# Performance work log

Measured on AMD Instinct MI355X. Metric: run time of the kernel, lower is better.

The kernel has to match this reference:

```python
import jax, jax.numpy as jnp
import numpy as np

# Physical constants and grid (match torch WRF.__init__)
PREF = 100000.0
RD = 287.0
G = 9.81
NX, NY, NZ = 384, 384, 48
DX, DY = 1000.0, 1000.0
DZ = 1.0 / (NZ + 1)

# --- staggered-grid stencil primitives (replace F.conv3d with shifts) ---

def pad_x(X):
    # periodic in x
    return jnp.concatenate([X[:, :, -1:], X, X[:, :, :1]], axis=2)

def pad_y(X):
    # periodic in y
    return jnp.concatenate([X[:, -1:, :], X, X[:, :1, :]], axis=1)

def pad_z(X, top=None, surface=None):
    # Dirichlet in z (defaults to zero boundary planes)
    top = top if top is not None else jnp.zeros_like(X[:1])
    surface = surface if surface is not None else jnp.zeros_like(X[:1])
    return jnp.concatenate([top, X, surface], axis=0)

def bar_x(X):
    return (X[:, :, 1:] + X[:, :, :-1]) * 0.5

def bar_y(X):
    return (X[:, 1:, :] + X[:, :-1, :]) * 0.5

def bar_z(X):
    return (X[1:] + X[:-1]) * 0.5

def delta_x(X):
    return (X[:, :, 1:] - X[:, :, :-1]) / DX

def delta_y(X):
    return (X[:, 1:, :] - X[:, :-1, :]) / DY

def delta_z(X):
    return (X[1:] - X[:-1]) / DZ


def rhs(U, V, W, Theta, Mu, Phi, Phi_t, Phi_s, P_t, P_s):
    u = U / bar_x(pad_x(Mu))                      # (NZ, NY, NX+1)
    v = V / bar_y(pad_y(Mu))                      # (NZ, NY+1, NX)
    w = W / bar_z(Mu)                             # (NZ-1, NY, NX)
    alpha = -delta_z(pad_z(Phi, Phi_t, Phi_s)) / Mu   # (NZ, NY, NX)
    theta = Theta / Mu
    p = PREF * (RD * theta / PREF / alpha) ** 1.4
    omega = -w * G / bar_z(alpha) / bar_z(Mu)     # (NZ-1, NY, NX)
    Omega = omega * bar_z(Mu)

    R_U = (-delta_x(bar_x(pad_x(U)) * bar_x(pad_x(u)))
           - delta_y(bar_x(pad_x(V)) * bar_y(pad_y(u)))
           - delta_z(bar_x(pad_x(pad_z(Omega))) * bar_z(pad_z(u))))
    R_V = (-delta_x(bar_y(pad_y(U)) * bar_x(pad_x(v)))
           - delta_y(bar_y(pad_y(V)) * bar_y(pad_y(v)))
           - delta_z(bar_y(pad_y(pad_z(Omega))) * bar_z(pad_z(v))))
    R_W = (-delta_x(bar_z(U) * bar_x(pad_x(w)))
           - delta_y(bar_z(V) * bar_y(pad_y(w)))
           - delta_z(bar_z(pad_z(Omega)) * bar_z(pad_z(w))))
    R_Theta = (-delta_x(U * bar_x(pad_x(theta)))
               - delta_y(V * bar_y(pad_y(theta)))
               - delta_z(pad_z(Omega) * bar_z(pad_z(theta))))
    R_Phi = (-bar_z(bar_x(u)) * delta_x(bar_x(pad_x(Phi)))
             - bar_z(bar_y(v)) * delta_y(bar_y(pad_y(Phi)))
             - omega * delta_z(bar_z(pad_z(Phi, Phi_t, Phi_s))))
    R_Mu = -delta_x(U) - delta_y(V) - delta_z(pad_z(Omega))

    # pressure-gradient terms
    R_U = R_U + (-bar_x(pad_x(Mu)) * bar_x(pad_x(alpha)) * delta_x(pad_x(p))
                 - delta_z(bar_x(bar_z(pad_x(pad_z(p, P_t, P_s)))))
                   * delta_x(pad_x(bar_z(pad_z(Phi, Phi_t, Phi_s)))))
    R_V = R_V + (-bar_y(pad_y(Mu)) * bar_y(pad_y(alpha)) * delta_y(pad_y(p))
                 - delta_z(bar_y(bar_z(pad_y(pad_z(p, P_t, P_s)))))
                   * delta_y(pad_y(bar_z(pad_z(Phi, Phi_t, Phi_s)))))
    R_W = R_W + G * (delta_z(p) - bar_z(Mu))
    R_Phi = R_Phi + G * w
    return R_U, R_V, R_W, R_Theta, R_Mu, R_Phi


def rk3_step(U, V, W, Theta, Mu, Phi, Phi_t, Phi_s, P_t, P_s, dt):
    Uc, Vc, Wc, Tc, Mc, Pc = U, V, W, Theta, Mu, Phi
    for c in (dt / 3.0, dt / 2.0, dt * 1.0):
        rU, rV, rW, rT, rM, rP = rhs(Uc, Vc, Wc, Tc, Mc, Pc, Phi_t, Phi_s, P_t, P_s)
        Uc = U + c * rU
        Vc = V + c * rV
        Wc = W + c * rW
        Tc = Theta + c * rT
        Mc = Mu + c * rM
        Pc = Phi + c * rP
    return (Uc, Vc, Wc, Tc, Mc, Pc)


def setup_inputs() -> dict:
    key = jax.random.key(0)
    k_th, k_u, k_v, k_w = jax.random.split(key, 4)
    # potential temperature with boundary layers, ~300 K
    theta_full = 300.0 + 0.5 * jax.random.normal(k_th, (NZ + 2, NY, NX), dtype=jnp.float32)
    P_t = jnp.zeros((1, NY, NX), dtype=jnp.float32)
    P_s = jnp.full((1, NY, NX), PREF, dtype=jnp.float32)
    # reproduce __init__ hydrostatic setup
    P = jnp.linspace(DZ, 1.0 - DZ, NZ, dtype=jnp.float32).reshape(NZ, 1, 1) * (P_s - P_t) + P_t
    Alpha = RD / PREF * theta_full[1:-1] * (P / PREF) ** (-1.0 / 1.4)
    Mu = jnp.broadcast_to(P_s - P_t, (NZ, NY, NX)).astype(jnp.float32)
    layer = Mu * Alpha * DZ                                  # (NZ, NY, NX)
    # Phi_full[i] = sum_{j>=i} layer[j], Phi_full[NZ] = 0
    Phi_full = jnp.concatenate(
        [jnp.flip(jnp.cumsum(jnp.flip(layer, 0), axis=0), 0),
         jnp.zeros((1, NY, NX), dtype=jnp.float32)], axis=0)  # (NZ+1, NY, NX)
    Phi_t = Phi_full[:1]
    Phi_s = Phi_full[-1:]
    Phi = Phi_full[1:-1]                                     # (NZ-1, NY, NX)
    Theta = theta_full[1:-1] * Mu
    U = 5e5 * jax.random.normal(k_u, (NZ, NY, NX + 1), dtype=jnp.float32)
    V = 5e5 * jax.random.normal(k_v, (NZ, NY + 1, NX), dtype=jnp.float32)
    W = 1e4 * jax.random.normal(k_w, (NZ - 1, NY, NX), dtype=jnp.float32)
    return {"U": U, "V": V, "W": W, "Theta": Theta, "Mu": Mu, "Phi": Phi,
            "Phi_t": Phi_t, "Phi_s": Phi_s, "P_t": P_t, "P_s": P_s, "dt": 4}


def reference(U, V, W, Theta, Mu, Phi, Phi_t, Phi_s, P_t, P_s, dt):
    return rk3_step(U, V, W, Theta, Mu, Phi, Phi_t, Phi_s, P_t, P_s, dt)
```

## Files before the change

kernel.cpp:

```cpp
#include <hip/hip_runtime.h>

namespace {

constexpr int NX = 384, NY = 384, NZ = 48;
constexpr int NXU = NX + 1;
constexpr int PLN = NX * NY;
constexpr float RDX = 1.0f / 1000.0f;
constexpr float RDY = 1.0f / 1000.0f;
constexpr float RDZ = 49.0f;
constexpr float PREF = 100000.0f, RD = 287.0f, G = 9.81f;
constexpr float K_RP = RD / PREF;

constexpr int SZ_U = NZ * NY * NXU;
constexpr int SZ_V = NZ * (NY + 1) * NX;
constexpr int SZ_W = (NZ - 1) * PLN;
constexpr int SZ_T = NZ * PLN;
constexpr int SZ_M = NZ * PLN;
constexpr int SZ_P = (NZ - 1) * PLN;

constexpr int TX = 32, TY = 8;
constexpr int PW = TX + 3;
constexpr int PH = TY + 3;
constexpr int PSZ = PW * PH;
constexpr int KCH = 12, KSPLIT = 4;

struct Idx { int pix, uo, vo, pxa, pxb, pya, pyb; };

__device__ __forceinline__ float frcp(float x) { return __builtin_amdgcn_rcpf(x); }
__device__ __forceinline__ float pow14(float x) {
    return __builtin_amdgcn_exp2f(1.4f * __builtin_amdgcn_logf(x));
}

__global__ __launch_bounds__(256, 3)
void rhs_tile(
    const float* __restrict__ Us, const float* __restrict__ Vs, const float* __restrict__ Ws,
    const float* __restrict__ Ts, const float* __restrict__ Ms, const float* __restrict__ Ps,
    const float* __restrict__ Phit, const float* __restrict__ Phis,
    const float* __restrict__ Pt,   const float* __restrict__ Psrf,
    const float* __restrict__ U0, const float* __restrict__ V0, const float* __restrict__ W0,
    const float* __restrict__ T0, const float* __restrict__ M0, const float* __restrict__ P0,
    float* __restrict__ Uo, float* __restrict__ Vo, float* __restrict__ Wo,
    float* __restrict__ To, float* __restrict__ Mo, float* __restrict__ Po,
    const int* __restrict__ dtp, float coef)
{
    const int tx = threadIdx.x, ty = threadIdx.y;
    const int tid = ty * TX + tx;
    const int i0 = blockIdx.x * TX;
    const int j0 = blockIdx.y * TY;
    const int k0 = blockIdx.z * KCH;
    const int i = i0 + tx, j = j0 + ty;
    const float c = coef * (float)(*dtp);
    const int ly = ty + 1, lx = tx + 1;

    __shared__ float sPH[3][PSZ], sP[3][PSZ], sOM[3][PSZ];
    __shared__ float sAL[2][PSZ], sMU[2][PSZ], sTH[2][PSZ], sUR[2][PSZ], su_[2][PSZ],
                     sVR[2][PSZ], sv_[2][PSZ], sw_[2][PSZ];

    auto mkidx = [&](int idx, Idx& q) {
        const int r  = idx / PW;
        const int cc = idx - r * PW;
        int gj = j0 - 1 + r;  if (gj < 0) gj += NY; else if (gj >= NY) gj -= NY;
        int gi = i0 - 1 + cc; if (gi < 0) gi += NX; else if (gi >= NX) gi -= NX;
        int gII = i0 - 1 + cc; if (gII < 0) gII += NX + 1; else if (gII > NX) gII -= NX + 1;
        int gJJ = j0 - 1 + r;  if (gJJ < 0) gJJ += NY + 1; else if (gJJ > NY) gJJ -= NY + 1;
        q.pix = gj * NX + gi;
        q.uo  = gj * NXU + gII;
        q.vo  = gJJ * NX + gi;
        const int xa = (gII == 0)  ? NX - 1 : gII - 1;
        const int xb = (gII == NX) ? 0      : gII;
        const int ya = (gJJ == 0)  ? NY - 1 : gJJ - 1;
        const int yb = (gJJ == NY) ? 0      : gJJ;
        q.pxa = gj * NX + xa; q.pxb = gj * NX + xb;
        q.pya = ya * NX + gi; q.pyb = yb * NX + gi;
    };
    const bool has2 = (tid + 256 < PSZ);
    Idx q0, q1;
    mkidx(tid, q0);
    mkidx(has2 ? tid + 256 : tid, q1);

    auto fill1 = [&](int l, const Idx& q, int idx) {
        const int s3 = (l + 3) % 3, s2 = l & 1;
        float phv, pv, al = 0.f, th = 0.f, uv = 0.f, vv = 0.f, wv = 0.f, om = 0.f;
        float Uw = 0.f, Vw = 0.f, muw = 0.f;
        if (l >= 0 && l < NZ) {
            phv = (l >= NZ - 1) ? Phis[q.pix] : Ps[l * PLN + q.pix];
            const float phm = (l == 0) ? Phit[q.pix] : Ps[(l - 1) * PLN + q.pix];
            const float mu  = Ms[l * PLN + q.pix];
            const float rmu = frcp(mu);
            al = -(phv - phm) * RDZ * rmu;
            th = Ts[l * PLN + q.pix] * rmu;
            pv = PREF * pow14(K_RP * th * frcp(al));
            const float Uv = Us[l * NY * NXU + q.uo];
            uv = Uv * frcp(0.5f * (Ms[l * PLN + q.pxa] + Ms[l * PLN + q.pxb]));
            const float Vv = Vs[l * (NY + 1) * NX + q.vo];
            vv = Vv * frcp(0.5f * (Ms[l * PLN + q.pya] + Ms[l * PLN + q.pyb]));
            Uw = Uv; Vw = Vv; muw = mu;
            if (l < NZ - 1) {
                const float mu1 = Ms[(l + 1) * PLN + q.pix];
                const float Wv  = Ws[l * PLN + q.pix];
                const float ph1 = (l + 1 >= NZ - 1) ? Phis[q.pix] : Ps[(l + 1) * PLN + q.pix];
                const float al1 = -(ph1 - phv) * RDZ * frcp(mu1);
                const float mz  = 0.5f * (mu + mu1);
                wv = Wv * frcp(mz);
                om = -Wv * G * frcp(0.5f * (al + al1) * mz);
            }
        } else {
            phv = (l < 0) ? Phit[q.pix] : Phis[q.pix];
            pv  = (l < 0) ? Pt[q.pix]   : Psrf[q.pix];
        }
        sPH[s3][idx] = phv; sP[s3][idx] = pv; sOM[s3][idx] = om;
        sAL[s2][idx] = al;  sMU[s2][idx] = muw; sTH[s2][idx] = th;
        sUR[s2][idx] = Uw;  su_[s2][idx] = uv;
        sVR[s2][idx] = Vw;  sv_[s2][idx] = vv;
        sw_[s2][idx] = wv;
    };
    auto fill = [&](int l) {
        fill1(l, q0, tid);
        if (has2) fill1(l, q1, tid + 256);
    };

    fill(k0 - 1);
    fill(k0);
    __syncthreads();

    const int e0 = (k0 - 1) & 1;
    float th_m  = sTH[e0][ly * PW + lx];
    float u_m   = su_[e0][ly * PW + lx];
    float u_m_e = su_[e0][ly * PW + lx + 1];
    float v_m   = sv_[e0][ly * PW + lx];
    float v_m_e = sv_[e0][(ly + 1) * PW + lx];
    float w_m   = sw_[e0][ly * PW + lx];

    for (int k = k0; k < k0 + KCH; ++k) {
        fill(k + 1);
        __syncthreads();

        const float* PHa = sPH[(k + 2) % 3];
        const float* PHb = sPH[k % 3];
        const float* PHc = sPH[(k + 1) % 3];
        const float* Pa  = sP[(k + 2) % 3];
        const float* Pb  = sP[k % 3];
        const float* Pc  = sP[(k + 1) % 3];
        const float* Oa  = sOM[(k + 2) % 3];
        const float* Ob  = sOM[k % 3];
        const float* Oc  = sOM[(k + 1) % 3];
        const int e = k & 1, f = (k + 1) & 1;
        const float* ALe = sAL[e];
        const float* MUe = sMU[e]; const float* MUf = sMU[f];
        const float* THe = sTH[e]; const float* THf = sTH[f];
        const float* URe = sUR[e]; const float* URf = sUR[f];
        const float* ue  = su_[e]; const float* uf  = su_[f];
        const float* VRe = sVR[e]; const float* VRf = sVR[f];
        const float* ve  = sv_[e]; const float* vf  = sv_[f];
        const float* we  = sw_[e]; const float* wf  = sw_[f];

        auto AT = [&](const float* p, int rr, int cc2) -> float { return p[rr * PW + cc2]; };

        auto R_U_c = [&](int cc, float ukm) -> float {
            const float u0 = AT(ue, ly, cc), um = AT(ue, ly, cc - 1), up = AT(ue, ly, cc + 1);
            const float Uc = AT(URe, ly, cc), Um = AT(URe, ly, cc - 1), Up = AT(URe, ly, cc + 1);
            float r = -0.25f * ((Uc + Up) * (u0 + up) - (Um + Uc) * (um + u0)) * RDX;
            const float VBj  = 0.5f * (AT(VRe, ly, cc - 1) + AT(VRe, ly, cc));
            const float VBj1 = 0.5f * (AT(VRe, ly + 1, cc - 1) + AT(VRe, ly + 1, cc));
            const float uS = AT(ue, ly - 1, cc), uN = AT(ue, ly + 1, cc);
            r -= (VBj1 * 0.5f * (u0 + uN) - VBj * 0.5f * (uS + u0)) * RDY;
            const float OBk  = 0.5f * (AT(Oa, ly, cc - 1) + AT(Oa, ly, cc));
            const float OBk1 = 0.5f * (AT(Ob, ly, cc - 1) + AT(Ob, ly, cc));
            const float ukp = AT(uf, ly, cc);
            r -= (OBk1 * 0.5f * (u0 + ukp) - OBk * 0.5f * (ukm + u0)) * RDZ;
            const float mux = 0.5f * (AT(MUe, ly, cc - 1) + AT(MUe, ly, cc));
            const float alx = 0.5f * (AT(ALe, ly, cc - 1) + AT(ALe, ly, cc));
            const float dpx = (AT(Pb, ly, cc) - AT(Pb, ly, cc - 1)) * RDX;
            r -= mux * alx * dpx;
            const float pzk  = 0.25f * (AT(Pa, ly, cc - 1) + AT(Pb, ly, cc - 1)
                                      + AT(Pa, ly, cc)     + AT(Pb, ly, cc));
            const float pzk1 = 0.25f * (AT(Pb, ly, cc - 1) + AT(Pc, ly, cc - 1)
                                      + AT(Pb, ly, cc)     + AT(Pc, ly, cc));
            const float dpz = (pzk1 - pzk) * RDZ;
            const float pza = 0.5f * (AT(PHa, ly, cc - 1) + AT(PHb, ly, cc - 1));
            const float pzb = 0.5f * (AT(PHa, ly, cc)     + AT(PHb, ly, cc));
            r -= dpz * (pzb - pza) * RDX;
            return r;
        };

        auto R_V_c = [&](int rr, float vkm) -> float {
            const float v0 = AT(ve, rr, lx), vm = AT(ve, rr - 1, lx), vp = AT(ve, rr + 1, lx);
            const float Vc = AT(VRe, rr, lx), Vm = AT(VRe, rr - 1, lx), Vp = AT(VRe, rr + 1, lx);
            float r = -0.25f * ((Vc + Vp) * (v0 + vp) - (Vm + Vc) * (vm + v0)) * RDY;
            const float UBi  = 0.5f * (AT(URe, rr - 1, lx)     + AT(URe, rr, lx));
            const float UBi1 = 0.5f * (AT(URe, rr - 1, lx + 1) + AT(URe, rr, lx + 1));
            const float vW = AT(ve, rr, lx - 1), vE = AT(ve, rr, lx + 1);
            r -= (UBi1 * 0.5f * (v0 + vE) - UBi * 0.5f * (vW + v0)) * RDX;
            const float OBk  = 0.5f * (AT(Oa, rr - 1, lx) + AT(Oa, rr, lx));
            const float OBk1 = 0.5f * (AT(Ob, rr - 1, lx) + AT(Ob, rr, lx));
            const float vkp = AT(vf, rr, lx);
            r -= (OBk1 * 0.5f * (v0 + vkp) - OBk * 0.5f * (vkm + v0)) * RDZ;
            const float muy = 0.5f * (AT(MUe, rr - 1, lx) + AT(MUe, rr, lx));
            const float aly = 0.5f * (AT(ALe, rr - 1, lx) + AT(ALe, rr, lx));
            const float dpy = (AT(Pb, rr, lx) - AT(Pb, rr - 1, lx)) * RDY;
            r -= muy * aly * dpy;
            const float pzk  = 0.25f * (AT(Pa, rr - 1, lx) + AT(Pb, rr - 1, lx)
                                      + AT(Pa, rr, lx)     + AT(Pb, rr, lx));
            const float pzk1 = 0.25f * (AT(Pb, rr - 1, lx) + AT(Pc, rr - 1, lx)
                                      + AT(Pb, rr, lx)     + AT(Pc, rr, lx));
            const float dpz = (pzk1 - pzk) * RDZ;
            const float pza = 0.5f * (AT(PHa, rr - 1, lx) + AT(PHb, rr - 1, lx));
            const float pzb = 0.5f * (AT(PHa, rr, lx)     + AT(PHb, rr, lx));
            r -= dpz * (pzb - pza) * RDY;
            return r;
        };

        const float th0 = AT(THe, ly, lx);
        float rT = -(AT(URe, ly, lx + 1) * 0.5f * (th0 + AT(THe, ly, lx + 1))
                   - AT(URe, ly, lx)     * 0.5f * (AT(THe, ly, lx - 1) + th0)) * RDX
                   -(AT(VRe, ly + 1, lx) * 0.5f * (th0 + AT(THe, ly + 1, lx))
                   - AT(VRe, ly, lx)     * 0.5f * (AT(THe, ly - 1, lx) + th0)) * RDY;
        const float th_p = AT(THf, ly, lx);
        const float Hk  = AT(Oa, ly, lx) * 0.5f * (th_m + th0);
        const float Hk1 = AT(Ob, ly, lx) * 0.5f * (th0 + th_p);
        rT -= (Hk1 - Hk) * RDZ;

        const float rM = -(AT(URe, ly, lx + 1) - AT(URe, ly, lx)) * RDX
                         -(AT(VRe, ly + 1, lx) - AT(VRe, ly, lx)) * RDY
                         -(AT(Ob, ly, lx) - AT(Oa, ly, lx)) * RDZ;

        const int idc = (k * NY + j) * NX + i;
        To[idc] = T0[idc] + c * rT;
        Mo[idc] = M0[idc] + c * rM;
        const int idu = (k * NY + j) * NXU + i;
        Uo[idu] = U0[idu] + c * R_U_c(lx, u_m);
        const int idv = (k * (NY + 1) + j) * NX + i;
        Vo[idv] = V0[idv] + c * R_V_c(ly, v_m);

        if (k < NZ - 1) {
            const float w0 = AT(we, ly, lx);
            const float Uzi  = 0.5f * (AT(URe, ly, lx)     + AT(URf, ly, lx));
            const float Uzi1 = 0.5f * (AT(URe, ly, lx + 1) + AT(URf, ly, lx + 1));
            const float wW = AT(we, ly, lx - 1), wE = AT(we, ly, lx + 1);
            float rW = -(Uzi1 * 0.5f * (w0 + wE) - Uzi * 0.5f * (wW + w0)) * RDX;
            const float Vzj  = 0.5f * (AT(VRe, ly, lx)     + AT(VRf, ly, lx));
            const float Vzj1 = 0.5f * (AT(VRe, ly + 1, lx) + AT(VRf, ly + 1, lx));
            const float wS = AT(we, ly - 1, lx), wN = AT(we, ly + 1, lx);
            rW -= (Vzj1 * 0.5f * (w0 + wN) - Vzj * 0.5f * (wS + w0)) * RDY;
            const float OZk  = 0.5f * (AT(Oa, ly, lx) + AT(Ob, ly, lx));
            const float OZk1 = 0.5f * (AT(Ob, ly, lx) + AT(Oc, ly, lx));
            const float wkp = AT(wf, ly, lx);
            rW -= (OZk1 * 0.5f * (w0 + wkp) - OZk * 0.5f * (w_m + w0)) * RDZ;
            const float muz = 0.5f * (AT(MUe, ly, lx) + AT(MUf, ly, lx));
            rW += G * ((AT(Pc, ly, lx) - AT(Pb, ly, lx)) * RDZ - muz);

            const float ubz = 0.25f * (AT(ue, ly, lx) + AT(ue, ly, lx + 1)
                                     + AT(uf, ly, lx) + AT(uf, ly, lx + 1));
            const float dfx = (AT(PHb, ly, lx + 1) - AT(PHb, ly, lx - 1)) * (0.5f * RDX);
            const float vbz = 0.25f * (AT(ve, ly, lx) + AT(ve, ly + 1, lx)
                                     + AT(vf, ly, lx) + AT(vf, ly + 1, lx));
            const float dfy = (AT(PHb, ly + 1, lx) - AT(PHb, ly - 1, lx)) * (0.5f * RDY);
            const float rmuz = frcp(muz);
            const float om   = AT(Ob, ly, lx) * rmuz;
            const float dfz  = (AT(PHc, ly, lx) - AT(PHa, ly, lx)) * (0.5f * RDZ);
            const float rP = -ubz * dfx - vbz * dfy - om * dfz + G * w0;

            Wo[idc] = W0[idc] + c * rW;
            Po[idc] = P0[idc] + c * rP;
        }

        if (i == NX - 1) {
            Uo[idu + 1] = U0[idu + 1] + c * R_U_c(lx + 1, u_m_e);
        }
        if (j == NY - 1) {
            const int idv2 = (k * (NY + 1) + NY) * NX + i;
            Vo[idv2] = V0[idv2] + c * R_V_c(ly + 1, v_m_e);
        }

        th_m  = th0;
        u_m   = AT(ue, ly, lx);
        u_m_e = AT(ue, ly, lx + 1);
        v_m   = AT(ve, ly, lx);
        v_m_e = AT(ve, ly + 1, lx);
        w_m   = AT(we, ly, lx);

        __syncthreads();
    }
}

}

extern "C" void kernel_launch(void* const* d_in, const int* in_sizes, int n_in,
                              void* d_out, int out_size, void* d_ws, size_t ws_size,
                              hipStream_t stream)
{
    (void)in_sizes; (void)n_in; (void)out_size; (void)ws_size;

    const float* U0   = (const float*)d_in[0];
    const float* V0   = (const float*)d_in[1];
    const float* W0   = (const float*)d_in[2];
    const float* T0   = (const float*)d_in[3];
    const float* M0   = (const float*)d_in[4];
    const float* P0   = (const float*)d_in[5];
    const float* Phit = (const float*)d_in[6];
    const float* Phis = (const float*)d_in[7];
    const float* Pt   = (const float*)d_in[8];
    const float* Psrf = (const float*)d_in[9];
    const int*   dtp  = (const int*)d_in[10];

    float* out = (float*)d_out;
    float* ws  = (float*)d_ws;

    float* outU = out;
    float* outV = outU + SZ_U;
    float* outW = outV + SZ_V;
    float* outT = outW + SZ_W;
    float* outM = outT + SZ_T;
    float* outP = outM + SZ_M;

    float* wsU = ws;
    float* wsV = wsU + SZ_U;
    float* wsW = wsV + SZ_V;
    float* wsT = wsW + SZ_W;
    float* wsM = wsT + SZ_T;
    float* wsP = wsM + SZ_M;

    const dim3 blk(TX, TY, 1);
    const dim3 grd(NX / TX, NY / TY, KSPLIT);

    const float coefs[3] = {1.0f / 3.0f, 0.5f, 1.0f};

    const float* sU[3] = {U0, outU, wsU};
    const float* sV[3] = {V0, outV, wsV};
    const float* sW[3] = {W0, outW, wsW};
    const float* sT[3] = {T0, outT, wsT};
    const float* sM[3] = {M0, outM, wsM};
    const float* sP_[3] = {P0, outP, wsP};
    float* oU[3] = {outU, wsU, outU};
    float* oV[3] = {outV, wsV, outV};
    float* oW[3] = {outW, wsW, outW};
    float* oT[3] = {outT, wsT, outT};
    float* oM[3] = {outM, wsM, outM};
    float* oP[3] = {outP, wsP, outP};

    for (int s = 0; s < 3; ++s) {
        rhs_tile<<<grd, blk, 0, stream>>>(
            sU[s], sV[s], sW[s], sT[s], sM[s], sP_[s],
            Phit, Phis, Pt, Psrf,
            U0, V0, W0, T0, M0, P0,
            oU[s], oV[s], oW[s], oT[s], oM[s], oP[s],
            dtp, coefs[s]);
    }
}
```

Before: 649.5 us.

## Software-prefetch next level's global loads into registers and carry vertical values

Splits the per-level shared-memory fill into a register preload stage and a derive stage. The loads for level k+2 are issued right after the barrier, so they overlap with the stencil compute for level k. Values for the level above (phi, mu, alpha) are carried in registers from one level to the next instead of being reloaded and recomputed. This hides global memory latency and removes redundant loads and reciprocals, at the cost of more registers per thread (two sets of prefetch structs), which could lower occupancy under launch_bounds(256,3).

```diff
diff --git a/kernel.cpp b/kernel.cpp
--- a/kernel.cpp
+++ b/kernel.cpp
@@ -24,7 +24,9 @@
 constexpr int PSZ = PW * PH;
 constexpr int KCH = 12, KSPLIT = 4;
 
-struct Idx { int pix, uo, vo, pxa, pxb, pya, pyb; };
+struct Idx  { int pix, uo, vo, pxa, pxb, pya, pyb; };
+struct Pref { float ph1, mu1, tht, Uv, Vv, Wv, mxa, mxb, mya, myb, phb, pb; };
+struct Carry{ float phc, muc, alc; };
 
 __device__ __forceinline__ float frcp(float x) { return __builtin_amdgcn_rcpf(x); }
 __device__ __forceinline__ float pow14(float x) {
@@ -78,35 +80,60 @@
     mkidx(tid, q0);
     mkidx(has2 ? tid + 256 : tid, q1);
 
-    auto fill1 = [&](int l, const Idx& q, int idx) {
+    auto preload = [&](int l, const Idx& q, Pref& P) {
+        if (l >= 0 && l < NZ) {
+            P.ph1 = (l + 2 >= NZ) ? Phis[q.pix] : Ps[(l + 1) * PLN + q.pix];
+            P.mu1 = (l + 1 < NZ) ? Ms[(l + 1) * PLN + q.pix] : 1.0f;
+            P.tht = Ts[l * PLN + q.pix];
+            P.Uv  = Us[l * NY * NXU + q.uo];
+            P.Vv  = Vs[l * (NY + 1) * NX + q.vo];
+            P.Wv  = (l < NZ - 1) ? Ws[l * PLN + q.pix] : 0.0f;
+            P.mxa = Ms[l * PLN + q.pxa]; P.mxb = Ms[l * PLN + q.pxb];
+            P.mya = Ms[l * PLN + q.pya]; P.myb = Ms[l * PLN + q.pyb];
+        } else if (l < 0) {
+            P.phb = Phit[q.pix]; P.pb = Pt[q.pix];
+            P.ph1 = Ps[q.pix];
+            P.mu1 = Ms[q.pix];
+        } else {
+            P.phb = Phis[q.pix]; P.pb = Psrf[q.pix];
+        }
+    };
+
+    auto initCarry = [&](int l, const Idx& q, Carry& C) {
+        C.phc = (l + 1 >= NZ) ? Phis[q.pix] : Ps[l * PLN + q.pix];
+        const float phm = (l == 0) ? Phit[q.pix] : Ps[(l - 1) * PLN + q.pix];
+        C.muc = Ms[l * PLN + q.pix];
+        C.alc = -(C.phc - phm) * RDZ * frcp(C.muc);
+    };
+
+    auto derive = [&](int l, const Pref& P, Carry& C, int idx) {
         const int s3 = (l + 3) % 3, s2 = l & 1;
         float phv, pv, al = 0.f, th = 0.f, uv = 0.f, vv = 0.f, wv = 0.f, om = 0.f;
         float Uw = 0.f, Vw = 0.f, muw = 0.f;
         if (l >= 0 && l < NZ) {
-            phv = (l >= NZ - 1) ? Phis[q.pix] : Ps[l * PLN + q.pix];
-            const float phm = (l == 0) ? Phit[q.pix] : Ps[(l - 1) * PLN + q.pix];
-            const float mu  = Ms[l * PLN + q.pix];
+            phv = C.phc;
+            const float mu = C.muc;
+            al = C.alc;
             const float rmu = frcp(mu);
-            al = -(phv - phm) * RDZ * rmu;
-            th = Ts[l * PLN + q.pix] * rmu;
+            th = P.tht * rmu;
             pv = PREF * pow14(K_RP * th * frcp(al));
-            const float Uv = Us[l * NY * NXU + q.uo];
-            uv = Uv * frcp(0.5f * (Ms[l * PLN + q.pxa] + Ms[l * PLN + q.pxb]));
-            const float Vv = Vs[l * (NY + 1) * NX + q.vo];
-            vv = Vv * frcp(0.5f * (Ms[l * PLN + q.pya] + Ms[l * PLN + q.pyb]));
-            Uw = Uv; Vw = Vv; muw = mu;
+            uv = P.Uv * frcp(0.5f * (P.mxa + P.mxb));
+            vv = P.Vv * frcp(0.5f * (P.mya + P.myb));
+            Uw = P.Uv; Vw = P.Vv; muw = mu;
+            float al1 = 0.f;
             if (l < NZ - 1) {
-                const float mu1 = Ms[(l + 1) * PLN + q.pix];
-                const float Wv  = Ws[l * PLN + q.pix];
-                const float ph1 = (l + 1 >= NZ - 1) ? Phis[q.pix] : Ps[(l + 1) * PLN + q.pix];
-                const float al1 = -(ph1 - phv) * RDZ * frcp(mu1);
-                const float mz  = 0.5f * (mu + mu1);
-                wv = Wv * frcp(mz);
-                om = -Wv * G * frcp(0.5f * (al + al1) * mz);
+                al1 = -(P.ph1 - phv) * RDZ * frcp(P.mu1);
+                const float mz = 0.5f * (mu + P.mu1);
+                wv = P.Wv * frcp(mz);
+                om = -P.Wv * G * frcp(0.5f * (al + al1) * mz);
             }
+            C.phc = P.ph1; C.muc = P.mu1; C.alc = al1;
+        } else if (l < 0) {
+            phv = P.phb; pv = P.pb;
+            const float al1 = -(P.ph1 - phv) * RDZ * frcp(P.mu1);
+            C.phc = P.ph1; C.muc = P.mu1; C.alc = al1;
         } else {
-            phv = (l < 0) ? Phit[q.pix] : Phis[q.pix];
-            pv  = (l < 0) ? Pt[q.pix]   : Psrf[q.pix];
+            phv = P.phb; pv = P.pb;
         }
         sPH[s3][idx] = phv; sP[s3][idx] = pv; sOM[s3][idx] = om;
         sAL[s2][idx] = al;  sMU[s2][idx] = muw; sTH[s2][idx] = th;
@@ -114,13 +141,13 @@
         sVR[s2][idx] = Vw;  sv_[s2][idx] = vv;
         sw_[s2][idx] = wv;
     };
-    auto fill = [&](int l) {
-        fill1(l, q0, tid);
-        if (has2) fill1(l, q1, tid + 256);
-    };
-
-    fill(k0 - 1);
-    fill(k0);
+
+    Pref p0, p1; Carry c0, c1;
+    if (k0 >= 1) { initCarry(k0 - 1, q0, c0); if (has2) initCarry(k0 - 1, q1, c1); }
+    preload(k0 - 1, q0, p0); if (has2) preload(k0 - 1, q1, p1);
+    derive(k0 - 1, p0, c0, tid); if (has2) derive(k0 - 1, p1, c1, tid + 256);
+    preload(k0, q0, p0); if (has2) preload(k0, q1, p1);
+    derive(k0, p0, c0, tid); if (has2) derive(k0, p1, c1, tid + 256);
     __syncthreads();
 
     const int e0 = (k0 - 1) & 1;
@@ -131,9 +158,17 @@
     float v_m_e = sv_[e0][(ly + 1) * PW + lx];
     float w_m   = sw_[e0][ly * PW + lx];
 
+    preload(k0 + 1, q0, p0); if (has2) preload(k0 + 1, q1, p1);
+
     for (int k = k0; k < k0 + KCH; ++k) {
-        fill(k + 1);
+        derive(k + 1, p0, c0, tid);
+        if (has2) derive(k + 1, p1, c1, tid + 256);
         __syncthreads();
+
+        if (k + 2 <= k0 + KCH) {
+            preload(k + 2, q0, p0);
+            if (has2) preload(k + 2, q1, p1);
+        }
 
         const float* PHa = sPH[(k + 2) % 3];
         const float* PHb = sPH[k % 3];
```

Result: slower. 810.5 us (+24.8%).

## Prefetch raw fields into LDS with async global_load_lds multi-level ring buffers

Applied to the files above, without the earlier changes.

Replaces the per-level direct global loads in the fill step with asynchronous global_load_lds copies of raw Phi, Mu, U, V, Theta and W into ring buffers several levels ahead. The derived quantities are then computed from LDS, and alpha is recomputed on the fly instead of being stored. The goal is to hide global-memory latency behind the stencil compute and to stop reloading neighbouring Mu from global memory. In exchange the kernel uses more complex indexing and LDS traffic, and it relies on the async copies having completed by the next barrier without explicit vmcnt waits, which risks races. It also leaves dead placeholder code behind (fillDirect).

```diff
diff --git a/kernel.cpp b/kernel.cpp
--- a/kernel.cpp
+++ b/kernel.cpp
@@ -8,8 +8,8 @@
 constexpr float RDX = 1.0f / 1000.0f;
 constexpr float RDY = 1.0f / 1000.0f;
 constexpr float RDZ = 49.0f;
-constexpr float PREF = 100000.0f, RD = 287.0f, G = 9.81f;
-constexpr float K_RP = RD / PREF;
+constexpr float PREF = 100000.0f, G = 9.81f;
+constexpr float K_RP = 287.0f / PREF;
 
 constexpr int SZ_U = NZ * NY * NXU;
 constexpr int SZ_V = NZ * (NY + 1) * NX;
@@ -22,14 +22,37 @@
 constexpr int PW = TX + 3;
 constexpr int PH = TY + 3;
 constexpr int PSZ = PW * PH;
+constexpr int WW = PW + 1;
+constexpr int WH = PH + 1;
+constexpr int WSZ = WW * WH;
+constexpr int ZP = 448;
 constexpr int KCH = 12, KSPLIT = 4;
 
-struct Idx { int pix, uo, vo, pxa, pxb, pya, pyb; };
+constexpr int O_PH = 0;
+constexpr int O_MS = O_PH + 5 * ZP;
+constexpr int O_UR = O_MS + 4 * ZP;
+constexpr int O_VR = O_UR + 3 * ZP;
+constexpr int O_TS = O_VR + 3 * ZP;
+constexpr int O_WS = O_TS + ZP;
+constexpr int O_P  = O_WS + ZP;
+constexpr int O_OM = O_P  + 3 * PSZ;
+constexpr int O_TH = O_OM + 3 * PSZ;
+constexpr int O_u  = O_TH + 2 * PSZ;
+constexpr int O_v  = O_u  + 2 * PSZ;
+constexpr int O_w  = O_v  + 2 * PSZ;
+constexpr int LTOT = O_w + 2 * PSZ;
 
 __device__ __forceinline__ float frcp(float x) { return __builtin_amdgcn_rcpf(x); }
 __device__ __forceinline__ float pow14(float x) {
     return __builtin_amdgcn_exp2f(1.4f * __builtin_amdgcn_logf(x));
 }
+__device__ __forceinline__ void gll4(const float* src, float* ldsWaveBase) {
+    __builtin_amdgcn_global_load_lds(
+        (const __attribute__((address_space(1))) void*)src,
+        (__attribute__((address_space(3))) void*)ldsWaveBase, 4, 0, 0);
+}
+__device__ __forceinline__ int imin(int a, int b) { return a < b ? a : b; }
+__device__ __forceinline__ int imax(int a, int b) { return a > b ? a : b; }
 
 __global__ __launch_bounds__(256, 3)
 void rhs_tile(
@@ -43,6 +66,8 @@
     float* __restrict__ To, float* __restrict__ Mo, float* __restrict__ Po,
     const int* __restrict__ dtp, float coef)
 {
+    __shared__ float L[LTOT];
+
     const int tx = threadIdx.x, ty = threadIdx.y;
     const int tid = ty * TX + tx;
     const int i0 = blockIdx.x * TX;
@@ -51,178 +76,267 @@
     const int i = i0 + tx, j = j0 + ty;
     const float c = coef * (float)(*dtp);
     const int ly = ty + 1, lx = tx + 1;
-
-    __shared__ float sPH[3][PSZ], sP[3][PSZ], sOM[3][PSZ];
-    __shared__ float sAL[2][PSZ], sMU[2][PSZ], sTH[2][PSZ], sUR[2][PSZ], su_[2][PSZ],
-                     sVR[2][PSZ], sv_[2][PSZ], sw_[2][PSZ];
-
-    auto mkidx = [&](int idx, Idx& q) {
-        const int r  = idx / PW;
-        const int cc = idx - r * PW;
+    const int wb = tid & ~63;
+    const bool w2 = (tid < 192);
+    const bool has2 = (tid + 256 < PSZ);
+
+    auto mkcell = [&](int idx, int& pix, int& uo, int& vo) {
+        const int r = idx / PW, cc = idx - r * PW;
         int gj = j0 - 1 + r;  if (gj < 0) gj += NY; else if (gj >= NY) gj -= NY;
         int gi = i0 - 1 + cc; if (gi < 0) gi += NX; else if (gi >= NX) gi -= NX;
         int gII = i0 - 1 + cc; if (gII < 0) gII += NX + 1; else if (gII > NX) gII -= NX + 1;
         int gJJ = j0 - 1 + r;  if (gJJ < 0) gJJ += NY + 1; else if (gJJ > NY) gJJ -= NY + 1;
-        q.pix = gj * NX + gi;
-        q.uo  = gj * NXU + gII;
-        q.vo  = gJJ * NX + gi;
-        const int xa = (gII == 0)  ? NX - 1 : gII - 1;
-        const int xb = (gII == NX) ? 0      : gII;
-        const int ya = (gJJ == 0)  ? NY - 1 : gJJ - 1;
-        const int yb = (gJJ == NY) ? 0      : gJJ;
-        q.pxa = gj * NX + xa; q.pxb = gj * NX + xb;
-        q.pya = ya * NX + gi; q.pyb = yb * NX + gi;
+        pix = gj * NX + gi; uo = gj * NXU + gII; vo = gJJ * NX + gi;
     };
-    const bool has2 = (tid + 256 < PSZ);
-    Idx q0, q1;
-    mkidx(tid, q0);
-    mkidx(has2 ? tid + 256 : tid, q1);
-
-    auto fill1 = [&](int l, const Idx& q, int idx) {
-        const int s3 = (l + 3) % 3, s2 = l & 1;
-        float phv, pv, al = 0.f, th = 0.f, uv = 0.f, vv = 0.f, wv = 0.f, om = 0.f;
-        float Uw = 0.f, Vw = 0.f, muw = 0.f;
+    auto mkwide = [&](int idxw, int& pixw) {
+        const int r = idxw / WW, cc = idxw - r * WW;
+        int gj = j0 - 2 + r;  if (gj < 0) gj += NY; else if (gj >= NY) gj -= NY;
+        int gi = i0 - 2 + cc; if (gi < 0) gi += NX; else if (gi >= NX) gi -= NX;
+        pixw = gj * NX + gi;
+    };
+    int pixA, uoA, voA, pixB, uoB, voB, pwA, pwB;
+    mkcell(tid, pixA, uoA, voA);
+    mkcell(imin(tid + 256, PSZ - 1), pixB, uoB, voB);
+    mkwide(tid, pwA);
+    mkwide(imin(tid + 256, WSZ - 1), pwB);
+
+    auto stage = [&](int k) {
+        {
+            const int m = k + 3;
+            const float* sA = (m >= NZ - 1) ? &Phis[pixA] : &Ps[m * PLN + pixA];
+            gll4(sA, &L[O_PH + (m % 5) * ZP + wb]);
+            if (w2) {
+                const float* sB = (m >= NZ - 1) ? &Phis[pixB] : &Ps[m * PLN + pixB];
+                gll4(sB, &L[O_PH + (m % 5) * ZP + wb + 256]);
+            }
+        }
+        {
+            const int lc = imin(k + 3, NZ - 1);
+            gll4(&Ms[lc * PLN + pwA], &L[O_MS + ((k + 3) % 4) * ZP + wb]);
+            if (w2) gll4(&Ms[lc * PLN + pwB], &L[O_MS + ((k + 3) % 4) * ZP + wb + 256]);
+        }
+        {
+            const int lc = imin(k + 2, NZ - 1);
+            gll4(&Us[lc * NY * NXU + uoA], &L[O_UR + ((k + 2) % 3) * ZP + wb]);
+            if (w2) gll4(&Us[lc * NY * NXU + uoB], &L[O_UR + ((k + 2) % 3) * ZP + wb + 256]);
+            gll4(&Vs[lc * (NY + 1) * NX + voA], &L[O_VR + ((k + 2) % 3) * ZP + wb]);
+            if (w2) gll4(&Vs[lc * (NY + 1) * NX + voB], &L[O_VR + ((k + 2) % 3) * ZP + wb + 256]);
+            gll4(&Ts[lc * PLN + pixA], &L[O_TS + wb]);
+            if (w2) gll4(&Ts[lc * PLN + pixB], &L[O_TS + wb + 256]);
+            const int lw = imin(k + 2, NZ - 2);
+            gll4(&Ws[lw * PLN + pixA], &L[O_WS + wb]);
+            if (w2) gll4(&Ws[lw * PLN + pixB], &L[O_WS + wb + 256]);
+        }
+    };
+
+    auto derive = [&](int l, int idx, int pix, float tsv, float wsv) {
+        const int r = idx / PW, cc = idx - r * PW;
+        const int wc = (r + 1) * WW + (cc + 1);
+        const int s3 = ((l % 3) + 3) % 3, s2 = l & 1;
+        float pv, th = 0.f, uv = 0.f, vv = 0.f, wv = 0.f, om = 0.f;
         if (l >= 0 && l < NZ) {
-            phv = (l >= NZ - 1) ? Phis[q.pix] : Ps[l * PLN + q.pix];
-            const float phm = (l == 0) ? Phit[q.pix] : Ps[(l - 1) * PLN + q.pix];
-            const float mu  = Ms[l * PLN + q.pix];
+            const int m4 = l % 4, m5 = l % 5, p5 = ((l - 1) % 5 + 5) % 5;
+            const float mu  = L[O_MS + m4 * ZP + wc];
+            const float phv = L[O_PH + m5 * ZP + idx];
+            const float phm = L[O_PH + p5 * ZP + idx];
             const float rmu = frcp(mu);
-            al = -(phv - phm) * RDZ * rmu;
-            th = Ts[l * PLN + q.pix] * rmu;
+            const float al  = -(phv - phm) * RDZ * rmu;
+            th = tsv * rmu;
             pv = PREF * pow14(K_RP * th * frcp(al));
-            const float Uv = Us[l * NY * NXU + q.uo];
-            uv = Uv * frcp(0.5f * (Ms[l * PLN + q.pxa] + Ms[l * PLN + q.pxb]));
-            const float Vv = Vs[l * (NY + 1) * NX + q.vo];
-            vv = Vv * frcp(0.5f * (Ms[l * PLN + q.pya] + Ms[l * PLN + q.pyb]));
-            Uw = Uv; Vw = Vv; muw = mu;
+            uv = L[O_UR + (l % 3) * ZP + idx]
+                 * frcp(0.5f * (L[O_MS + m4 * ZP + wc - 1] + L[O_MS + m4 * ZP + wc]));
+            vv = L[O_VR + (l % 3) * ZP + idx]
+                 * frcp(0.5f * (L[O_MS + m4 * ZP + wc - WW] + L[O_MS + m4 * ZP + wc]));
             if (l < NZ - 1) {
-                const float mu1 = Ms[(l + 1) * PLN + q.pix];
-                const float Wv  = Ws[l * PLN + q.pix];
-                const float ph1 = (l + 1 >= NZ - 1) ? Phis[q.pix] : Ps[(l + 1) * PLN + q.pix];
+                const float mu1 = L[O_MS + ((l + 1) % 4) * ZP + wc];
+                const float ph1 = L[O_PH + ((l + 1) % 5) * ZP + idx];
                 const float al1 = -(ph1 - phv) * RDZ * frcp(mu1);
                 const float mz  = 0.5f * (mu + mu1);
-                wv = Wv * frcp(mz);
-                om = -Wv * G * frcp(0.5f * (al + al1) * mz);
+                wv = wsv * frcp(mz);
+                om = -wsv * G * frcp(0.5f * (al + al1) * mz);
             }
         } else {
-            phv = (l < 0) ? Phit[q.pix] : Phis[q.pix];
-            pv  = (l < 0) ? Pt[q.pix]   : Psrf[q.pix];
-        }
-        sPH[s3][idx] = phv; sP[s3][idx] = pv; sOM[s3][idx] = om;
-        sAL[s2][idx] = al;  sMU[s2][idx] = muw; sTH[s2][idx] = th;
-        sUR[s2][idx] = Uw;  su_[s2][idx] = uv;
-        sVR[s2][idx] = Vw;  sv_[s2][idx] = vv;
-        sw_[s2][idx] = wv;
+            pv = (l < 0) ? Pt[pix] : Psrf[pix];
+        }
+        L[O_P  + s3 * PSZ + idx] = pv;
+        L[O_OM + s3 * PSZ + idx] = om;
+        L[O_TH + s2 * PSZ + idx] = th;
+        L[O_u  + s2 * PSZ + idx] = uv;
+        L[O_v  + s2 * PSZ + idx] = vv;
+        L[O_w  + s2 * PSZ + idx] = wv;
     };
-    auto fill = [&](int l) {
-        fill1(l, q0, tid);
-        if (has2) fill1(l, q1, tid + 256);
-    };
-
-    fill(k0 - 1);
-    fill(k0);
+
+    {
+        auto fillDirect = [&](int idx, int pix, int uo, int vo, int pixw, bool doW) {
+            for (int m = k0 - 2; m <= k0 + 2; ++m) {
+                float v = (m >= NZ - 1) ? Phis[pix] : ((m < 0) ? Phit[pix] : Ps[m * PLN + pix]);
+                L[O_PH + ((m % 5 + 5) % 5) * ZP + idx] = v;
+            }
+            if (doW) {
+                for (int l = k0 - 1; l <= k0 + 2; ++l) {
+                    const int lc = imin(imax(l, 0), NZ - 1);
+                    L[O_MS + ((l % 4 + 4) % 4) * ZP + pixw == pixw ? 0 : 0];
+                }
+            }
+            (void)uo; (void)vo;
+        };
+        (void)fillDirect;
+        for (int m = k0 - 2; m <= k0 + 2; ++m) {
+            float v = (m >= NZ - 1) ? Phis[pixA] : ((m < 0) ? Phit[pixA] : Ps[m * PLN + pixA]);
+            L[O_PH + ((m % 5 + 5) % 5) * ZP + tid] = v;
+        }
+        for (int l = k0 - 1; l <= k0 + 2; ++l) {
+            const int lc = imin(imax(l, 0), NZ - 1);
+            L[O_MS + ((l % 4 + 4) % 4) * ZP + tid] = Ms[lc * PLN + pwA];
+        }
+        for (int l = k0 - 1; l <= k0 + 1; ++l) {
+            const int lc = imin(imax(l, 0), NZ - 1);
+            L[O_UR + ((l % 3 + 3) % 3) * ZP + tid] = Us[lc * NY * NXU + uoA];
+            L[O_VR + ((l % 3 + 3) % 3) * ZP + tid] = Vs[lc * (NY + 1) * NX + voA];
+        }
+        if (has2) {
+            const int idx = tid + 256;
+            for (int m = k0 - 2; m <= k0 + 2; ++m) {
+                float v = (m >= NZ - 1) ? Phis[pixB] : ((m < 0) ? Phit[pixB] : Ps[m * PLN + pixB]);
+                L[O_PH + ((m % 5 + 5) % 5) * ZP + idx] = v;
+            }
+            for (int l = k0 - 1; l <= k0 + 1; ++l) {
+                const int lc = imin(imax(l, 0), NZ - 1);
+                L[O_UR + ((l % 3 + 3) % 3) * ZP + idx] = Us[lc * NY * NXU + uoB];
+                L[O_VR + ((l % 3 + 3) % 3) * ZP + idx] = Vs[lc * (NY + 1) * NX + voB];
+            }
+        }
+        if (tid + 256 < WSZ) {
+            const int idx = tid + 256;
+            for (int l = k0 - 1; l <= k0 + 2; ++l) {
+                const int lc = imin(imax(l, 0), NZ - 1);
+                L[O_MS + ((l % 4 + 4) % 4) * ZP + idx] = Ms[lc * PLN + pwB];
+            }
+        }
+    }
     __syncthreads();
 
+    {
+        int lc = imin(imax(k0 - 1, 0), NZ - 1), lw = imin(imax(k0 - 1, 0), NZ - 2);
+        derive(k0 - 1, tid, pixA, Ts[lc * PLN + pixA], Ws[lw * PLN + pixA]);
+        if (has2) derive(k0 - 1, tid + 256, pixB, Ts[lc * PLN + pixB], Ws[lw * PLN + pixB]);
+        lc = imin(k0, NZ - 1); lw = imin(k0, NZ - 2);
+        derive(k0, tid, pixA, Ts[lc * PLN + pixA], Ws[lw * PLN + pixA]);
+        if (has2) derive(k0, tid + 256, pixB, Ts[lc * PLN + pixB], Ws[lw * PLN + pixB]);
+    }
+    {
+        const int lc = imin(k0 + 1, NZ - 1), lw = imin(k0 + 1, NZ - 2);
+        gll4(&Ts[lc * PLN + pixA], &L[O_TS + wb]);
+        if (w2) gll4(&Ts[lc * PLN + pixB], &L[O_TS + wb + 256]);
+        gll4(&Ws[lw * PLN + pixA], &L[O_WS + wb]);
+        if (w2) gll4(&Ws[lw * PLN + pixB], &L[O_WS + wb + 256]);
+    }
+    __syncthreads();
+
     const int e0 = (k0 - 1) & 1;
-    float th_m  = sTH[e0][ly * PW + lx];
-    float u_m   = su_[e0][ly * PW + lx];
-    float u_m_e = su_[e0][ly * PW + lx + 1];
-    float v_m   = sv_[e0][ly * PW + lx];
-    float v_m_e = sv_[e0][(ly + 1) * PW + lx];
-    float w_m   = sw_[e0][ly * PW + lx];
+    float th_m  = L[O_TH + e0 * PSZ + ly * PW + lx];
+    float u_m   = L[O_u  + e0 * PSZ + ly * PW + lx];
+    float u_m_e = L[O_u  + e0 * PSZ + ly * PW + lx + 1];
+    float v_m   = L[O_v  + e0 * PSZ + (ly + 1) * PW + lx - PW + PW];
+    float v_m_  = L[O_v  + e0 * PSZ + ly * PW + lx];
+    float v_m_e = L[O_v  + e0 * PSZ + (ly + 1) * PW + lx];
+    float w_m   = L[O_w  + e0 * PSZ + ly * PW + lx];
+    v_m = v_m_;
 
     for (int k = k0; k < k0 + KCH; ++k) {
-        fill(k + 1);
+        derive(k + 1, tid, pixA, L[O_TS + tid], L[O_WS + tid]);
+        if (has2) derive(k + 1, tid + 256, pixB, L[O_TS + tid + 256], L[O_WS + tid + 256]);
         __syncthreads();
 
-        const float* PHa = sPH[(k + 2) % 3];
-        const float* PHb = sPH[k % 3];
-        const float* PHc = sPH[(k + 1) % 3];
-        const float* Pa  = sP[(k + 2) % 3];
-        const float* Pb  = sP[k % 3];
-        const float* Pc  = sP[(k + 1) % 3];
-        const float* Oa  = sOM[(k + 2) % 3];
-        const float* Ob  = sOM[k % 3];
-        const float* Oc  = sOM[(k + 1) % 3];
-        const int e = k & 1, f = (k + 1) & 1;
-        const float* ALe = sAL[e];
-        const float* MUe = sMU[e]; const float* MUf = sMU[f];
-        const float* THe = sTH[e]; const float* THf = sTH[f];
-        const float* URe = sUR[e]; const float* URf = sUR[f];
-        const float* ue  = su_[e]; const float* uf  = su_[f];
-        const float* VRe = sVR[e]; const float* VRf = sVR[f];
-        const float* ve  = sv_[e]; const float* vf  = sv_[f];
-        const float* we  = sw_[e]; const float* wf  = sw_[f];
-
-        auto AT = [&](const float* p, int rr, int cc2) -> float { return p[rr * PW + cc2]; };
+        stage(k);
+
+        const int a5 = (k + 4) % 5, b5 = k % 5, c5 = (k + 1) % 5;
+        const int aP = (k + 2) % 3, bP = k % 3, cP = (k + 1) % 3;
+        const int m4 = k % 4, n4 = (k + 1) % 4;
+        const int e = k & 1, f = 1 - e;
+        const int eU = k % 3, fU = (k + 1) % 3;
+
+        auto PHx = [&](int s, int rr, int cc) { return L[O_PH + s * ZP + rr * PW + cc]; };
+        auto Px  = [&](int s, int rr, int cc) { return L[O_P  + s * PSZ + rr * PW + cc]; };
+        auto Ox  = [&](int s, int rr, int cc) { return L[O_OM + s * PSZ + rr * PW + cc]; };
+        auto MUx = [&](int s, int rr, int cc) { return L[O_MS + s * ZP + (rr + 1) * WW + cc + 1]; };
+        auto THx = [&](int s, int rr, int cc) { return L[O_TH + s * PSZ + rr * PW + cc]; };
+        auto URx = [&](int s, int rr, int cc) { return L[O_UR + s * ZP + rr * PW + cc]; };
+        auto VRx = [&](int s, int rr, int cc) { return L[O_VR + s * ZP + rr * PW + cc]; };
+        auto ux  = [&](int s, int rr, int cc) { return L[O_u  + s * PSZ + rr * PW + cc]; };
+        auto vx  = [&](int s, int rr, int cc) { return L[O_v  + s * PSZ + rr * PW + cc]; };
+        auto wx  = [&](int s, int rr, int cc) { return L[O_w  + s * PSZ + rr * PW + cc]; };
+        auto ALk = [&](int rr, int cc) {
+            return -(PHx(b5, rr, cc) - PHx(a5, rr, cc)) * RDZ * frcp(MUx(m4, rr, cc));
+        };
 
         auto R_U_c = [&](int cc, float ukm) -> float {
-            const float u0 = AT(ue, ly, cc), um = AT(ue, ly, cc - 1), up = AT(ue, ly, cc + 1);
-            const float Uc = AT(URe, ly, cc), Um = AT(URe, ly, cc - 1), Up = AT(URe, ly, cc + 1);
+            const float u0 = ux(e, ly, cc), um = ux(e, ly, cc - 1), up = ux(e, ly, cc + 1);
+            const float Uc = URx(eU, ly, cc), Um = URx(eU, ly, cc - 1), Up = URx(eU, ly, cc + 1);
             float r = -0.25f * ((Uc + Up) * (u0 + up) - (Um + Uc) * (um + u0)) * RDX;
-            const float VBj  = 0.5f * (AT(VRe, ly, cc - 1) + AT(VRe, ly, cc));
-            const float VBj1 = 0.5f * (AT(VRe, ly + 1, cc - 1) + AT(VRe, ly + 1, cc));
-            const float uS = AT(ue, ly - 1, cc), uN = AT(ue, ly + 1, cc);
+            const float VBj  = 0.5f * (VRx(eU, ly, cc - 1) + VRx(eU, ly, cc));
+            const float VBj1 = 0.5f * (VRx(eU, ly + 1, cc - 1) + VRx(eU, ly + 1, cc));
+            const float uS = ux(e, ly - 1, cc), uN = ux(e, ly + 1, cc);
             r -= (VBj1 * 0.5f * (u0 + uN) - VBj * 0.5f * (uS + u0)) * RDY;
-            const float OBk  = 0.5f * (AT(Oa, ly, cc - 1) + AT(Oa, ly, cc));
-            const float OBk1 = 0.5f * (AT(Ob, ly, cc - 1) + AT(Ob, ly, cc));
-            const float ukp = AT(uf, ly, cc);
+            const float OBk  = 0.5f * (Ox(aP, ly, cc - 1) + Ox(aP, ly, cc));
+            const float OBk1 = 0.5f * (Ox(bP, ly, cc - 1) + Ox(bP, ly, cc));
+            const float ukp = ux(f, ly, cc);
             r -= (OBk1 * 0.5f * (u0 + ukp) - OBk * 0.5f * (ukm + u0)) * RDZ;
-            const float mux = 0.5f * (AT(MUe, ly, cc - 1) + AT(MUe, ly, cc));
-            const float alx = 0.5f * (AT(ALe, ly, cc - 1) + AT(ALe, ly, cc));
-            const float dpx = (AT(Pb, ly, cc) - AT(Pb, ly, cc - 1)) * RDX;
-            r -= mux * alx * dpx;
-            const float pzk  = 0.25f * (AT(Pa, ly, cc - 1) + AT(Pb, ly, cc - 1)
-                                      + AT(Pa, ly, cc)     + AT(Pb, ly, cc));
-            const float pzk1 = 0.25f * (AT(Pb, ly, cc - 1) + AT(Pc, ly, cc - 1)
-                                      + AT(Pb, ly, cc)     + AT(Pc, ly, cc));
+            const float mux_ = 0.5f * (MUx(m4, ly, cc - 1) + MUx(m4, ly, cc));
+            const float alx  = 0.5f * (ALk(ly, cc - 1) + ALk(ly, cc));
+            const float dpx  = (Px(bP, ly, cc) - Px(bP, ly, cc - 1)) * RDX;
+            r -= mux_ * alx * dpx;
+            const float pzk  = 0.25f * (Px(aP, ly, cc - 1) + Px(bP, ly, cc - 1)
+                                      + Px(aP, ly, cc)     + Px(bP, ly, cc));
+            const float pzk1 = 0.25f * (Px(bP, ly, cc - 1) + Px(cP, ly, cc - 1)
+                                      + Px(bP, ly, cc)     + Px(cP, ly, cc));
             const float dpz = (pzk1 - pzk) * RDZ;
-            const float pza = 0.5f * (AT(PHa, ly, cc - 1) + AT(PHb, ly, cc - 1));
-            const float pzb = 0.5f * (AT(PHa, ly, cc)     + AT(PHb, ly, cc));
+            const float pza = 0.5f * (PHx(a5, ly, cc - 1) + PHx(b5, ly, cc - 1));
+            const float pzb = 0.5f * (PHx(a5, ly, cc)     + PHx(b5, ly, cc));
             r -= dpz * (pzb - pza) * RDX;
             return r;
         };
 
         auto R_V_c = [&](int rr, float vkm) -> float {
-            const float v0 = AT(ve, rr, lx), vm = AT(ve, rr - 1, lx), vp = AT(ve, rr + 1, lx);
-            const float Vc = AT(VRe, rr, lx), Vm = AT(VRe, rr - 1, lx), Vp = AT(VRe, rr + 1, lx);
+            const float v0 = vx(e, rr, lx), vm = vx(e, rr - 1, lx), vp = vx(e, rr + 1, lx);
+            const float Vc = VRx(eU, rr, lx), Vm = VRx(eU, rr - 1, lx), Vp = VRx(eU, rr + 1, lx);
             float r = -0.25f * ((Vc + Vp) * (v0 + vp) - (Vm + Vc) * (vm + v0)) * RDY;
-            const float UBi  = 0.5f * (AT(URe, rr - 1, lx)     + AT(URe, rr, lx));
-            const float UBi1 = 0.5f * (AT(URe, rr - 1, lx + 1) + AT(URe, rr, lx + 1));
-            const float vW = AT(ve, rr, lx - 1), vE = AT(ve, rr, lx + 1);
+            const float UBi  = 0.5f * (URx(eU, rr - 1, lx)     + URx(eU, rr, lx));
+            const float UBi1 = 0.5f * (URx(eU, rr - 1, lx + 1) + URx(eU, rr, lx + 1));
+            const float vW = vx(e, rr, lx - 1), vE = vx(e, rr, lx + 1);
             r -= (UBi1 * 0.5f * (v0 + vE) - UBi * 0.5f * (vW + v0)) * RDX;
-            const float OBk  = 0.5f * (AT(Oa, rr - 1, lx) + AT(Oa, rr, lx));
-            const float OBk1 = 0.5f * (AT(Ob, rr - 1, lx) + AT(Ob, rr, lx));
-            const float vkp = AT(vf, rr, lx);
+            const float OBk  = 0.5f * (Ox(aP, rr - 1, lx) + Ox(aP, rr, lx));
+            const float OBk1 = 0.5f * (Ox(bP, rr - 1, lx) + Ox(bP, rr, lx));
+            const float vkp = vx(f, rr, lx);
             r -= (OBk1 * 0.5f * (v0 + vkp) - OBk * 0.5f * (vkm + v0)) * RDZ;
-            const float muy = 0.5f * (AT(MUe, rr - 1, lx) + AT(MUe, rr, lx));
-            const float aly = 0.5f * (AT(ALe, rr - 1, lx) + AT(ALe, rr, lx));
-            const float dpy = (AT(Pb, rr, lx) - AT(Pb, rr - 1, lx)) * RDY;
+            const float muy = 0.5f * (MUx(m4, rr - 1, lx) + MUx(m4, rr, lx));
+            const float aly = 0.5f * (ALk(rr - 1, lx) + ALk(rr, lx));
+            const float dpy = (Px(bP, rr, lx) - Px(bP, rr - 1, lx)) * RDY;
             r -= muy * aly * dpy;
-            const float pzk  = 0.25f * (AT(Pa, rr - 1, lx) + AT(Pb, rr - 1, lx)
-                                      + AT(Pa, rr, lx)     + AT(Pb, rr, lx));
-            const float pzk1 = 0.25f * (AT(Pb, rr - 1, lx) + AT(Pc, rr - 1, lx)
-                                      + AT(Pb, rr, lx)     + AT(Pc, rr, lx));
+            const float pzk  = 0.25f * (Px(aP, rr - 1, lx) + Px(bP, rr - 1, lx)
+                                      + Px(aP, rr, lx)     + Px(bP, rr, lx));
+            const float pzk1 = 0.25f * (Px(bP, rr - 1, lx) + Px(cP, rr - 1, lx)
+                                      + Px(bP, rr, lx)     + Px(cP, rr, lx));
             const float dpz = (pzk1 - pzk) * RDZ;
-            const float pza = 0.5f * (AT(PHa, rr - 1, lx) + AT(PHb, rr - 1, lx));
-            const float pzb = 0.5f * (AT(PHa, rr, lx)     + AT(PHb, rr, lx));
+            const float pza = 0.5f * (PHx(a5, rr - 1, lx) + PHx(b5, rr - 1, lx));
+            const float pzb = 0.5f * (PHx(a5, rr, lx)     + PHx(b5, rr, lx));
             r -= dpz * (pzb - pza) * RDY;
             return r;
         };
 
-        const float th0 = AT(THe, ly, lx);
-        float rT = -(AT(URe, ly, lx + 1) * 0.5f * (th0 + AT(THe, ly, lx + 1))
-                   - AT(URe, ly, lx)     * 0.5f * (AT(THe, ly, lx - 1) + th0)) * RDX
-                   -(AT(VRe, ly + 1, lx) * 0.5f * (th0 + AT(THe, ly + 1, lx))
-                   - AT(VRe, ly, lx)     * 0.5f * (AT(THe, ly - 1, lx) + th0)) * RDY;
-        const float th_p = AT(THf, ly, lx);
-        const float Hk  = AT(Oa, ly, lx) * 0.5f * (th_m + th0);
-        const float Hk1 = AT(Ob, ly, lx) * 0.5f * (th0 + th_p);
+        const float th0 = THx(e, ly, lx);
+        float rT = -(URx(eU, ly, lx + 1) * 0.5f * (th0 + THx(e, ly, lx + 1))
+                   - URx(eU, ly, lx)     * 0.5f * (THx(e, ly, lx - 1) + th0)) * RDX
+                   -(VRx(eU, ly + 1, lx) * 0.5f * (th0 + THx(e, ly + 1, lx))
+                   - VRx(eU, ly, lx)     * 0.5f * (THx(e, ly - 1, lx) + th0)) * RDY;
+        const float th_p = THx(f, ly, lx);
+        const float Hk  = Ox(aP, ly, lx) * 0.5f * (th_m + th0);
+        const float Hk1 = Ox(bP, ly, lx) * 0.5f * (th0 + th_p);
         rT -= (Hk1 - Hk) * RDZ;
 
-        const float rM = -(AT(URe, ly, lx + 1) - AT(URe, ly, lx)) * RDX
-                         -(AT(VRe, ly + 1, lx) - AT(VRe, ly, lx)) * RDY
-                         -(AT(Ob, ly, lx) - AT(Oa, ly, lx)) * RDZ;
+        const float rM = -(URx(eU, ly, lx + 1) - URx(eU, ly, lx)) * RDX
+                         -(VRx(eU, ly + 1, lx) - VRx(eU, ly, lx)) * RDY
+                         -(Ox(bP, ly, lx) - Ox(aP, ly, lx)) * RDZ;
 
         const int idc = (k * NY + j) * NX + i;
         To[idc] = T0[idc] + c * rT;
@@ -233,31 +347,31 @@
         Vo[idv] = V0[idv] + c * R_V_c(ly, v_m);
 
         if (k < NZ - 1) {
-            const float w0 = AT(we, ly, lx);
-            const float Uzi  = 0.5f * (AT(URe, ly, lx)     + AT(URf, ly, lx));
-            const float Uzi1 = 0.5f * (AT(URe, ly, lx + 1) + AT(URf, ly, lx + 1));
-            const float wW = AT(we, ly, lx - 1), wE = AT(we, ly, lx + 1);
+            const float w0 = wx(e, ly, lx);
+            const float Uzi  = 0.5f * (URx(eU, ly, lx)     + URx(fU, ly, lx));
+            const float Uzi1 = 0.5f * (URx(eU, ly, lx + 1) + URx(fU, ly, lx + 1));
+            const float wW = wx(e, ly, lx - 1), wE = wx(e, ly, lx + 1);
             float rW = -(Uzi1 * 0.5f * (w0 + wE) - Uzi * 0.5f * (wW + w0)) * RDX;
-            const float Vzj  = 0.5f * (AT(VRe, ly, lx)     + AT(VRf, ly, lx));
-            const float Vzj1 = 0.5f * (AT(VRe, ly + 1, lx) + AT(VRf, ly + 1, lx));
-            const float wS = AT(we, ly - 1, lx), wN = AT(we, ly + 1, lx);
+            const float Vzj  = 0.5f * (VRx(eU, ly, lx)     + VRx(fU, ly, lx));
+            const float Vzj1 = 0.5f * (VRx(eU, ly + 1, lx) + VRx(fU, ly + 1, lx));
+            const float wS = wx(e, ly - 1, lx), wN = wx(e, ly + 1, lx);
             rW -= (Vzj1 * 0.5f * (w0 + wN) - Vzj * 0.5f * (wS + w0)) * RDY;
-            const float OZk  = 0.5f * (AT(Oa, ly, lx) + AT(Ob, ly, lx));
-            const float OZk1 = 0.5f * (AT(Ob, ly, lx) + AT(Oc, ly, lx));
-            const float wkp = AT(wf, ly, lx);
+            const float OZk  = 0.5f * (Ox(aP, ly, lx) + Ox(bP, ly, lx));
+            const float OZk1 = 0.5f * (Ox(bP, ly, lx) + Ox(cP, ly, lx));
+            const float wkp = wx(f, ly, lx);
             rW -= (OZk1 * 0.5f * (w0 + wkp) - OZk * 0.5f * (w_m + w0)) * RDZ;
-            const float muz = 0.5f * (AT(MUe, ly, lx) + AT(MUf, ly, lx));
-            rW += G * ((AT(Pc, ly, lx) - AT(Pb, ly, lx)) * RDZ - muz);
-
-            const float ubz = 0.25f * (AT(ue, ly, lx) + AT(ue, ly, lx + 1)
-                                     + AT(uf, ly, lx) + AT(uf, ly, lx + 1));
-            const float dfx = (AT(PHb, ly, lx + 1) - AT(PHb, ly, lx - 1)) * (0.5f * RDX);
-            const float vbz = 0.25f * (AT(ve, ly, lx) + AT(ve, ly + 1, lx)
-                                     + AT(vf, ly, lx) + AT(vf, ly + 1, lx));
-            const float dfy = (AT(PHb, ly + 1, lx) - AT(PHb, ly - 1, lx)) * (0.5f * RDY);
+            const float muz = 0.5f * (MUx(m4, ly, lx) + MUx(n4, ly, lx));
+            rW += G * ((Px(cP, ly, lx) - Px(bP, ly, lx)) * RDZ - muz);
+
+            const float ubz = 0.25f * (ux(e, ly, lx) + ux(e, ly, lx + 1)
+                                     + ux(f, ly, lx) + ux(f, ly, lx + 1));
+            const float dfx = (PHx(b5, ly, lx + 1) - PHx(b5, ly, lx - 1)) * (0.5f * RDX);
+            const float vbz = 0.25f * (vx(e, ly, lx) + vx(e, ly + 1, lx)
+                                     + vx(f, ly, lx) + vx(f, ly + 1, lx));
+            const float dfy = (PHx(b5, ly + 1, lx) - PHx(b5, ly - 1, lx)) * (0.5f * RDY);
             const float rmuz = frcp(muz);
-            const float om   = AT(Ob, ly, lx) * rmuz;
-            const float dfz  = (AT(PHc, ly, lx) - AT(PHa, ly, lx)) * (0.5f * RDZ);
+            const float om   = Ox(bP, ly, lx) * rmuz;
+            const float dfz  = (PHx(c5, ly, lx) - PHx(a5, ly, lx)) * (0.5f * RDZ);
             const float rP = -ubz * dfx - vbz * dfy - om * dfz + G * w0;
 
             Wo[idc] = W0[idc] + c * rW;
@@ -273,11 +387,11 @@
         }
 
         th_m  = th0;
-        u_m   = AT(ue, ly, lx);
-        u_m_e = AT(ue, ly, lx + 1);
-        v_m   = AT(ve, ly, lx);
-        v_m_e = AT(ve, ly + 1, lx);
-        w_m   = AT(we, ly, lx);
+        u_m   = ux(e, ly, lx);
+        u_m_e = ux(e, ly, lx + 1);
+        v_m   = vx(e, ly, lx);
+        v_m_e = vx(e, ly + 1, lx);
+        w_m   = wx(e, ly, lx);
 
         __syncthreads();
     }
```

Result: faster. 606.8 us (-6.6%).
